# Kernel optimization log

Hardware: AMD Instinct MI355X
Metric: run time of the kernel (lower is better)

## Reference

```python
import jax, jax.numpy as jnp
import numpy as np

HEADS = 8
DIM_HEAD = 64
NH = 16
NW = 16
SCALE = DIM_HEAD ** -0.5


def _avg2x2(a):
    # 2x2 average pool, stride 1, over axes 1,2 of [B,H,W,C] (== unfold+mean in torch)
    return (a[:, :-1, :-1] + a[:, 1:, :-1] + a[:, :-1, 1:] + a[:, 1:, 1:]) * 0.25


def _split_heads(t):
    B, n, _ = t.shape
    return t.reshape(B, n, HEADS, DIM_HEAD).transpose(0, 2, 1, 3)  # b h n d


def setup_inputs() -> dict:
    key = jax.random.key(0)
    ks = jax.random.split(key, 5)
    B, n, dim = 64, 482, 512
    inner = HEADS * DIM_HEAD
    return {
        "x": jax.random.normal(ks[0], (B, n, dim), jnp.float32),
        "mask": jax.random.normal(ks[1], (B, n, dim), jnp.float32),
        "W_qkv": jax.random.normal(ks[2], (3 * inner, dim), jnp.float32) * 0.02,
        "W_out": jax.random.normal(ks[3], (dim, inner), jnp.float32) * 0.02,
        "b_out": jax.random.normal(ks[4], (dim,), jnp.float32) * 0.02,
    }


def reference(x, mask, W_qkv, W_out, b_out):
    sg = jax.lax.stop_gradient
    B, n, dim = x.shape
    inner = HEADS * DIM_HEAD
    nHW = NH * NW            # 256
    nb = (NH - 1) * (NW - 1)  # 225

    # qkv projection
    qkv = x @ W_qkv.T                              # [B,n,3*inner]
    q, k, v = (
        _split_heads(t) for t in jnp.split(qkv, 3, axis=-1)
    )

    # mask path (no grad)
    mask_ = sg(mask)
    updated = (jnp.mean(mask_[:, 1:], axis=-1, keepdims=True) > 0.0).astype(x.dtype)
    updated = jnp.concatenate([jnp.ones_like(updated[:, :1]), updated], axis=1)  # [B,n,1]
    qkv_m = mask_ @ jnp.abs(sg(W_qkv)).T
    q_m, k_m, v_m = (_split_heads(t) for t in jnp.split(qkv_m, 3, axis=-1))
    q_m = q_m / (1e-6 + jnp.max(q_m, axis=2, keepdims=True))
    k_m = k_m / (1e-6 + jnp.max(k_m, axis=2, keepdims=True))
    v_m = v_m / (1e-6 + jnp.max(v_m, axis=2, keepdims=True))
    q_m, k_m, v_m = sg(q_m), sg(k_m), sg(v_m)

    # mask-modulated attention
    dots = jnp.einsum('bhnd,bhmd->bhnm', q * q_m, k * k_m) * SCALE
    attn = jax.nn.softmax(dots, axis=-1)
    out = jnp.einsum('bhnm,bhmd->bhnd', attn, v_m * v)
    out = out.transpose(0, 2, 1, 3).reshape(B, n, inner) * updated

    m = jnp.einsum('bhnm,bhmd->bhnd', sg(attn), v_m)
    m = sg(m.transpose(0, 2, 1, 3).reshape(B, n, inner) * updated)

    # overlap blending (is_overlap=True)
    inv_tail = 1.0 - updated[:, -nb:]
    inv_grid = 1.0 - updated[:, 1:nHW + 1]

    out_bridge = _avg2x2(out[:, 1:nHW + 1].reshape(B, NH, NW, inner)).reshape(B, nb, inner) * inv_tail
    out_origin = jnp.pad(out[:, -nb:].reshape(B, NH - 1, NW - 1, inner),
                         ((0, 0), (1, 1), (1, 1), (0, 0)))
    out_origin = _avg2x2(out_origin).reshape(B, nHW, inner) * inv_grid

    m_bridge = _avg2x2(m[:, 1:nHW + 1].reshape(B, NH, NW, inner)).reshape(B, nb, inner) * inv_tail
    m_origin = jnp.pad(m[:, -nb:].reshape(B, NH - 1, NW - 1, inner),
                       ((0, 0), (1, 1), (1, 1), (0, 0)))
    m_origin = _avg2x2(m_origin).reshape(B, nHW, inner) * inv_grid

    out = out.at[:, 1:nHW + 1].add(out_origin).at[:, -nb:].add(out_bridge)
    m = sg(m.at[:, 1:nHW + 1].add(m_origin).at[:, -nb:].add(m_bridge))

    # nearest-neighbor interpolation of mask means (no grad)
    mm = jnp.mean(m[:, 1:], axis=-1, keepdims=True)          # [B,n-1,1]
    a = mm[:, :nHW].reshape(B, 1, NH, NW)
    inter = jnp.repeat(jnp.repeat(a, 16, axis=2), 16, axis=3)  # [B,1,256,256]
    b = mm[:, -nb:].reshape(B, 1, NH - 1, NW - 1)
    inter_shift = jnp.repeat(jnp.repeat(b, 16, axis=2), 16, axis=3)  # [B,1,240,240]
    inter = inter.at[:, :, 8:-8, 8:-8].set((inter[:, :, 8:-8, 8:-8] + inter_shift) * 0.5)
    inter = sg(inter)

    m = sg(m @ jnp.abs(sg(W_out)).T)

    out_final = out @ W_out.T + b_out
    return out_final, m, inter
```

## Files before the change

kernel.cpp:

```cpp
#include <hip/hip_runtime.h>

#define B_      64
#define NSEQ    482
#define DIM     512
#define HEADS_  8
#define HD      64
#define QKV3    1536
#define NPAD    512
#define MROWS   (B_ * NSEQ)
#define GT      4096

typedef __bf16 v8bf __attribute__((ext_vector_type(8)));
typedef float  v4f  __attribute__((ext_vector_type(4)));
typedef unsigned int v4u __attribute__((ext_vector_type(4)));

typedef __attribute__((address_space(1))) const unsigned short gu16;
typedef __attribute__((address_space(3))) unsigned short lu16;

__device__ __forceinline__ unsigned short f2bf(float f) {
    unsigned u = __float_as_uint(f);
    u += 0x7fffu + ((u >> 16) & 1u);
    return (unsigned short)(u >> 16);
}
__device__ __forceinline__ float bf2f(unsigned short h) {
    return __uint_as_float(((unsigned)h) << 16);
}
__device__ __forceinline__ v8bf vabs8(v8bf x) {
    v4u u;
    __builtin_memcpy(&u, &x, 16);
    u &= (v4u){0x7fff7fffu, 0x7fff7fffu, 0x7fff7fffu, 0x7fff7fffu};
    v8bf r;
    __builtin_memcpy(&r, &u, 16);
    return r;
}

__global__ void k_cvt(const float* __restrict__ s, unsigned short* __restrict__ d, int n4) {
    int i = blockIdx.x * 256 + threadIdx.x;
    if (i < n4) {
        float4 v = ((const float4*)s)[i];
        ushort4 o;
        o.x = f2bf(v.x); o.y = f2bf(v.y); o.z = f2bf(v.z); o.w = f2bf(v.w);
        ((ushort4*)d)[i] = o;
    }
}

__global__ __launch_bounds__(256) void k_cvtmask(const float* __restrict__ mask,
                                                 unsigned short* __restrict__ mb,
                                                 float* __restrict__ upd) {
    int row = blockIdx.x * 4 + (threadIdx.x >> 6);
    int lane = threadIdx.x & 63;
    const float4* p = (const float4*)(mask + (size_t)row * DIM);
    ushort4* d = (ushort4*)(mb + (size_t)row * DIM);
    float s = 0.f;
    #pragma unroll
    for (int j = 0; j < 2; j++) {
        float4 v = p[j * 64 + lane];
        ushort4 o;
        o.x = f2bf(v.x); o.y = f2bf(v.y); o.z = f2bf(v.z); o.w = f2bf(v.w);
        d[j * 64 + lane] = o;
        s += v.x + v.y + v.z + v.w;
    }
    #pragma unroll
    for (int off = 32; off; off >>= 1) s += __shfl_xor(s, off);
    if (lane == 0) {
        int i = row % NSEQ;
        upd[row] = (i == 0) ? 1.f : ((s > 0.f) ? 1.f : 0.f);
    }
}

__global__ __launch_bounds__(256, 2) void k_gemm2(const unsigned short* __restrict__ A1,
                                                  const unsigned short* __restrict__ A2,
                                                  const unsigned short* __restrict__ Bw,
                                                  unsigned short* __restrict__ C1b,
                                                  unsigned short* __restrict__ C2b,
                                                  float* __restrict__ C1f,
                                                  float* __restrict__ C2f,
                                                  const float* __restrict__ bias,
                                                  int N, int K) {
    __shared__ __align__(16) unsigned short As1[3 * GT];
    __shared__ __align__(16) unsigned short As2[3 * GT];
    __shared__ __align__(16) unsigned short Bs[3 * GT];
    int tid = threadIdx.x;
    int lane = tid & 63, w = tid >> 6;
    int wm = w & 1, wn = w >> 1;
    int quad = lane >> 4, m16 = lane & 15;

    int nbx = gridDim.x, nwg = nbx * gridDim.y;
    int id = blockIdx.y * nbx + blockIdx.x;
    int q = nwg >> 3, r = nwg & 7;
    int xcd = id & 7, sub = id >> 3;
    int nid = (xcd < r ? xcd * (q + 1) : r * (q + 1) + (xcd - r) * q) + sub;
    int m0 = (nid / nbx) * 128, n0 = (nid % nbx) * 128;

    int srow = w * 16 + (lane >> 2);
    int scol = ((lane & 3) ^ ((lane >> 2) & 3)) * 8;
    const unsigned short* gA10 = &A1[(size_t)(m0 + srow) * K + scol];
    const unsigned short* gA11 = &A1[(size_t)(m0 + 64 + srow) * K + scol];
    const unsigned short* gA20 = &A2[(size_t)(m0 + srow) * K + scol];
    const unsigned short* gA21 = &A2[(size_t)(m0 + 64 + srow) * K + scol];
    const unsigned short* gB0  = &Bw[(size_t)(n0 + srow) * K + scol];
    const unsigned short* gB1  = &Bw[(size_t)(n0 + 64 + srow) * K + scol];
    lu16* lA10 = (lu16*)&As1[w * 512];
    lu16* lA11 = (lu16*)&As1[2048 + w * 512];
    lu16* lA20 = (lu16*)&As2[w * 512];
    lu16* lA21 = (lu16*)&As2[2048 + w * 512];
    lu16* lB0  = (lu16*)&Bs[w * 512];
    lu16* lB1  = (lu16*)&Bs[2048 + w * 512];

    v4f acc1[4][4], acc2[4][4];
    #pragma unroll
    for (int i = 0; i < 4; i++)
        #pragma unroll
        for (int j = 0; j < 4; j++) {
            acc1[i][j] = (v4f){0.f, 0.f, 0.f, 0.f};
            acc2[i][j] = (v4f){0.f, 0.f, 0.f, 0.f};
        }

    auto STAGE = [&](int bo, int s) {
        int ko = s << 5;
        __builtin_amdgcn_global_load_lds((gu16*)(gA10 + ko), lA10 + bo, 16, 0, 0);
        __builtin_amdgcn_global_load_lds((gu16*)(gA11 + ko), lA11 + bo, 16, 0, 0);
        __builtin_amdgcn_global_load_lds((gu16*)(gA20 + ko), lA20 + bo, 16, 0, 0);
        __builtin_amdgcn_global_load_lds((gu16*)(gA21 + ko), lA21 + bo, 16, 0, 0);
        __builtin_amdgcn_global_load_lds((gu16*)(gB0  + ko), lB0  + bo, 16, 0, 0);
        __builtin_amdgcn_global_load_lds((gu16*)(gB1  + ko), lB1  + bo, 16, 0, 0);
    };
    int csw = (quad ^ (m16 & 3)) << 3;
    auto COMPUTE = [&](int bo) {
        v8bf a1[4], a2[4];
        #pragma unroll
        for (int i = 0; i < 4; i++) {
            a1[i] = *(const v8bf*)&As1[bo + (wm * 64 + i * 16 + m16) * 32 + csw];
            a2[i] = *(const v8bf*)&As2[bo + (wm * 64 + i * 16 + m16) * 32 + csw];
        }
        #pragma unroll
        for (int j = 0; j < 4; j++) {
            v8bf bf = *(const v8bf*)&Bs[bo + (wn * 64 + j * 16 + m16) * 32 + csw];
            v8bf ba = vabs8(bf);
            #pragma unroll
            for (int i = 0; i < 4; i++) {
                acc1[i][j] = __builtin_amdgcn_mfma_f32_16x16x32_bf16(a1[i], bf, acc1[i][j], 0, 0, 0);
                acc2[i][j] = __builtin_amdgcn_mfma_f32_16x16x32_bf16(a2[i], ba, acc2[i][j], 0, 0, 0);
            }
        }
    };

    int steps = K >> 5;
    STAGE(0, 0);
    STAGE(GT, 1);
    int b0 = 0, b1 = GT, b2 = 2 * GT;
    for (int s = 0; s < steps; ++s) {
        if (s < steps - 1) asm volatile("s_waitcnt vmcnt(6)" ::: "memory");
        else               asm volatile("s_waitcnt vmcnt(0)" ::: "memory");
        __builtin_amdgcn_s_barrier();
        __builtin_amdgcn_sched_barrier(0);
        if (s + 2 < steps) STAGE(b2, s + 2);
        COMPUTE(b0);
        int t = b0; b0 = b1; b1 = b2; b2 = t;
    }
    __syncthreads();

    if (C1f) {
        #pragma unroll
        for (int j = 0; j < 4; j++) {
            int col = n0 + wn * 64 + j * 16 + m16;
            float bi = bias ? bias[col] : 0.f;
            #pragma unroll
            for (int i = 0; i < 4; i++) {
                int rowb = m0 + wm * 64 + i * 16 + quad * 4;
                #pragma unroll
                for (int r = 0; r < 4; r++) {
                    size_t off = (size_t)(rowb + r) * N + col;
                    C1f[off] = acc1[i][j][r] + bi;
                    C2f[off] = acc2[i][j][r];
                }
            }
        }
    } else {
        unsigned short* wbuf = &As1[w * 1024];
        int rr = lane >> 2;
        int c0 = ((lane & 3) * 2) ^ ((rr >> 1) & 7);
        size_t colb = n0 + wn * 64 + (lane & 3) * 16;
        #pragma unroll
        for (int i = 0; i < 4; i++) {
            #pragma unroll
            for (int j = 0; j < 4; j++)
                #pragma unroll
                for (int r = 0; r < 4; r++) {
                    int row = quad * 4 + r;
                    int e = j * 16 + m16;
                    int es = ((((e >> 3) ^ ((row >> 1) & 7)) << 3) | (e & 7));
                    wbuf[row * 64 + es] = f2bf(acc1[i][j][r]);
                }
            int4 p0 = *(const int4*)&wbuf[rr * 64 + c0 * 8];
            int4 p1 = *(const int4*)&wbuf[rr * 64 + (c0 ^ 1) * 8];
            size_t off0 = (size_t)(m0 + wm * 64 + i * 16 + rr) * N + colb;
            *(int4*)&C1b[off0] = p0;
            *(int4*)&C1b[off0 + 8] = p1;
        }
        #pragma unroll
        for (int i = 0; i < 4; i++) {
            #pragma unroll
            for (int j = 0; j < 4; j++)
                #pragma unroll
                for (int r = 0; r < 4; r++) {
                    int row = quad * 4 + r;
                    int e = j * 16 + m16;
                    int es = ((((e >> 3) ^ ((row >> 1) & 7)) << 3) | (e & 7));
                    wbuf[row * 64 + es] = f2bf(acc2[i][j][r]);
                }
            int4 p0 = *(const int4*)&wbuf[rr * 64 + c0 * 8];
            int4 p1 = *(const int4*)&wbuf[rr * 64 + (c0 ^ 1) * 8];
            size_t off0 = (size_t)(m0 + wm * 64 + i * 16 + rr) * N + colb;
            *(int4*)&C2b[off0] = p0;
            *(int4*)&C2b[off0 + 8] = p1;
        }
    }
}

__global__ void k_colmax(const unsigned short* __restrict__ qm, float* __restrict__ invsc) {
    int b = blockIdx.x;
    int c = blockIdx.y * 256 + threadIdx.x;
    const unsigned short* p = qm + (size_t)b * NSEQ * QKV3 + c;
    float mx = -1e30f;
    for (int i = 0; i < NSEQ; i++) mx = fmaxf(mx, bf2f(p[(size_t)i * QKV3]));
    invsc[b * QKV3 + c] = 1.f / (1e-6f + mx);
}

__global__ __launch_bounds__(256) void k_build(const unsigned short* __restrict__ qkv,
                                               const unsigned short* __restrict__ qm,
                                               const float* __restrict__ invsc,
                                               unsigned short* __restrict__ QQ,
                                               unsigned short* __restrict__ KK,
                                               unsigned short* __restrict__ VVt,
                                               unsigned short* __restrict__ VMt) {
    __shared__ unsigned short tv[64][72];
    __shared__ unsigned short tm[64][72];
    int tid = threadIdx.x;
    int dd = tid & 63, il = tid >> 6;
    int it = blockIdx.x, h = blockIdx.y, b = blockIdx.z;
    int i0 = it * 64;
    size_t bh = (size_t)(b * HEADS_ + h);
    int c = h * HD + dd;
    float invq = invsc[b * QKV3 + c] * 0.125f;
    float invk = invsc[b * QKV3 + 512 + c];
    float invv = invsc[b * QKV3 + 1024 + c];
    #pragma unroll 4
    for (int p = 0; p < 16; p++) {
        int li = p * 4 + il;
        int i = i0 + li;
        unsigned short oq = 0, ok = 0, ov = 0, om = 0;
        if (i < NSEQ) {
            size_t base = ((size_t)(b * NSEQ + i)) * QKV3 + c;
            float q  = bf2f(qkv[base]),        qv = bf2f(qm[base]);
            float kk = bf2f(qkv[base + 512]),  kv = bf2f(qm[base + 512]);
            float vv = bf2f(qkv[base + 1024]), vm = bf2f(qm[base + 1024]);
            oq = f2bf(q * qv * invq);
            ok = f2bf(kk * kv * invk);
            float vmn = vm * invv;
            ov = f2bf(vv * vmn);
            om = f2bf(vmn);
        }
        QQ[(bh * NPAD + i) * HD + dd] = oq;
        KK[(bh * NPAD + i) * HD + dd] = ok;
        tv[li][dd] = ov;
        tm[li][dd] = om;
    }
    __syncthreads();
    #pragma unroll 4
    for (int p = 0; p < 16; p++) {
        int dr = p * 4 + il;
        VVt[(bh * HD + dr) * NPAD + i0 + dd] = tv[dd][dr];
        VMt[(bh * HD + dr) * NPAD + i0 + dd] = tm[dd][dr];
    }
}

__global__ __launch_bounds__(256, 3) void k_attn(const unsigned short* __restrict__ QQ,
                                                 const unsigned short* __restrict__ KK,
                                                 const unsigned short* __restrict__ VVt,
                                                 const unsigned short* __restrict__ VMt,
                                                 const float* __restrict__ upd,
                                                 float* __restrict__ OUT1,
                                                 float* __restrict__ M1) {
    __shared__ __align__(16) unsigned short Ks[2][32 * 72];
    __shared__ __align__(16) unsigned short Vs[2][64 * 40];
    __shared__ __align__(16) unsigned short Ms[2][64 * 40];
    __shared__ __align__(16) unsigned short Ps[4][32 * 40];

    int tid = threadIdx.x;
    int w = tid >> 6, lane = tid & 63;
    int quad = lane >> 4, m16 = lane & 15;
    int id = (blockIdx.z * 8 + blockIdx.y) * 4 + blockIdx.x;
    int nid = (id & 7) * 256 + (id >> 3);
    int b = nid >> 5, h = (nid >> 2) & 7;
    int q0 = (nid & 3) * 128 + w * 32;
    size_t bh = (size_t)(b * HEADS_ + h);

    v8bf aq[2][2];
    #pragma unroll
    for (int s = 0; s < 2; s++) {
        const unsigned short* qb = &QQ[(bh * NPAD + q0 + s * 16 + m16) * HD];
        aq[s][0] = *(const v8bf*)&qb[quad * 8];
        aq[s][1] = *(const v8bf*)&qb[32 + quad * 8];
    }

    v4f vacc[2][4], macc[2][4];
    #pragma unroll
    for (int s = 0; s < 2; s++)
        #pragma unroll
        for (int dt = 0; dt < 4; dt++) {
            vacc[s][dt] = (v4f){0.f, 0.f, 0.f, 0.f};
            macc[s][dt] = (v4f){0.f, 0.f, 0.f, 0.f};
        }
    float lrun[2][4];
    #pragma unroll
    for (int s = 0; s < 2; s++)
        #pragma unroll
        for (int r = 0; r < 4; r++) lrun[s][r] = 0.f;

    const unsigned short* gK = &KK[bh * NPAD * HD + tid * 8];
    const unsigned short* gV = &VVt[(bh * HD + (tid >> 2)) * NPAD + (tid & 3) * 8];
    const unsigned short* gM = &VMt[(bh * HD + (tid >> 2)) * NPAD + (tid & 3) * 8];
    int oK = (tid >> 3) * 72 + (tid & 7) * 8;
    int oV = (tid >> 2) * 40 + (tid & 3) * 8;
    unsigned short* Pw = &Ps[w][0];

    int4 rk = *(const int4*)gK;
    int4 rv = *(const int4*)gV;
    int4 rm = *(const int4*)gM;

    for (int ic = 0; ic < 16; ++ic) {
        int buf = ic & 1;
        *(int4*)&Ks[buf][oK] = rk;
        *(int4*)&Vs[buf][oV] = rv;
        *(int4*)&Ms[buf][oV] = rm;
        if (ic < 15) {
            rk = *(const int4*)(gK + (ic + 1) * 32 * HD);
            rv = *(const int4*)(gV + (ic + 1) * 32);
            rm = *(const int4*)(gM + (ic + 1) * 32);
        }
        __syncthreads();

        v8bf kf[2][2];
        #pragma unroll
        for (int t = 0; t < 2; t++) {
            kf[t][0] = *(const v8bf*)&Ks[buf][(t * 16 + m16) * 72 + quad * 8];
            kf[t][1] = *(const v8bf*)&Ks[buf][(t * 16 + m16) * 72 + 32 + quad * 8];
        }
        v4f S[2][2];
        #pragma unroll
        for (int s = 0; s < 2; s++)
            #pragma unroll
            for (int t = 0; t < 2; t++) {
                v4f a = (v4f){0.f, 0.f, 0.f, 0.f};
                a = __builtin_amdgcn_mfma_f32_16x16x32_bf16(aq[s][0], kf[t][0], a, 0, 0, 0);
                a = __builtin_amdgcn_mfma_f32_16x16x32_bf16(aq[s][1], kf[t][1], a, 0, 0, 0);
                S[s][t] = a;
            }

        int i0 = ic * 32;
        if (i0 + 32 > NSEQ) {
            bool x0 = (i0 + m16) >= NSEQ;
            bool x1 = (i0 + 16 + m16) >= NSEQ;
            #pragma unroll
            for (int s = 0; s < 2; s++)
                #pragma unroll
                for (int r = 0; r < 4; r++) {
                    if (x0) S[s][0][r] = -1e30f;
                    if (x1) S[s][1][r] = -1e30f;
                }
        }

        #pragma unroll
        for (int s = 0; s < 2; s++)
            #pragma unroll
            for (int r = 0; r < 4; r++) {
                float e0 = __expf(S[s][0][r]);
                float e1 = __expf(S[s][1][r]);
                lrun[s][r] += e0 + e1;
                Pw[(s * 16 + quad * 4 + r) * 40 + m16] = f2bf(e0);
                Pw[(s * 16 + quad * 4 + r) * 40 + 16 + m16] = f2bf(e1);
            }

        v8bf ap[2];
        ap[0] = *(const v8bf*)&Pw[m16 * 40 + quad * 8];
        ap[1] = *(const v8bf*)&Pw[(16 + m16) * 40 + quad * 8];

        #pragma unroll
        for (int dt = 0; dt < 4; dt++) {
            v8bf bv = *(const v8bf*)&Vs[buf][(dt * 16 + m16) * 40 + quad * 8];
            v8bf bm = *(const v8bf*)&Ms[buf][(dt * 16 + m16) * 40 + quad * 8];
            #pragma unroll
            for (int s = 0; s < 2; s++) {
                vacc[s][dt] = __builtin_amdgcn_mfma_f32_16x16x32_bf16(ap[s], bv, vacc[s][dt], 0, 0, 0);
                macc[s][dt] = __builtin_amdgcn_mfma_f32_16x16x32_bf16(ap[s], bm, macc[s][dt], 0, 0, 0);
            }
        }
    }

    #pragma unroll
    for (int s = 0; s < 2; s++)
        #pragma unroll
        for (int r = 0; r < 4; r++) {
            float sum = lrun[s][r];
            sum += __shfl_xor(sum, 1);
            sum += __shfl_xor(sum, 2);
            sum += __shfl_xor(sum, 4);
            sum += __shfl_xor(sum, 8);
            float iv = 1.f / sum;
            int iq = q0 + s * 16 + quad * 4 + r;
            if (iq < NSEQ) {
                float u = upd[b * NSEQ + iq] * iv;
                size_t off = ((size_t)(b * NSEQ + iq)) * DIM + h * HD + m16;
                #pragma unroll
                for (int dt = 0; dt < 4; dt++) {
                    OUT1[off + dt * 16] = vacc[s][dt][r] * u;
                    M1[off + dt * 16]   = macc[s][dt][r] * u;
                }
            }
        }
}

__global__ __launch_bounds__(256) void k_blend(const float* __restrict__ O1,
                                               const float* __restrict__ Mm,
                                               const float* __restrict__ upd,
                                               unsigned short* __restrict__ O2,
                                               unsigned short* __restrict__ M2,
                                               float* __restrict__ mm) {
    int blk = blockIdx.x;
    int b = blk / NSEQ, i = blk - b * NSEQ;
    int tid = threadIdx.x;
    size_t rb = (size_t)blk * DIM;
    int ns = 0;
    size_t src[4];
    float wgt = 0.f;
    if (i >= 1) {
        wgt = 0.25f * (1.f - upd[blk]);
        if (wgt != 0.f) {
            if (i <= 256) {
                int g = i - 1, gy = g >> 4, gx = g & 15;
                #pragma unroll
                for (int dy = 0; dy < 2; dy++)
                    #pragma unroll
                    for (int dx = 0; dx < 2; dx++) {
                        int sy = gy - 1 + dy, sx = gx - 1 + dx;
                        if (sy >= 0 && sy < 15 && sx >= 0 && sx < 15)
                            src[ns++] = ((size_t)(b * NSEQ + 257 + sy * 15 + sx)) * DIM;
                    }
            } else {
                int t = i - 257, ty = t / 15, tx = t - ty * 15;
                #pragma unroll
                for (int dy = 0; dy < 2; dy++)
                    #pragma unroll
                    for (int dx = 0; dx < 2; dx++)
                        src[ns++] = ((size_t)(b * NSEQ + 1 + (ty + dy) * 16 + (tx + dx))) * DIM;
            }
        }
    }
    float msum = 0.f;
    for (int c = tid; c < DIM; c += 256) {
        float o = O1[rb + c], m = Mm[rb + c];
        float ao = 0.f, am = 0.f;
        for (int s = 0; s < ns; s++) { ao += O1[src[s] + c]; am += Mm[src[s] + c]; }
        o += wgt * ao;
        m += wgt * am;
        O2[rb + c] = f2bf(o);
        M2[rb + c] = f2bf(m);
        msum += m;
    }
    #pragma unroll
    for (int off = 32; off; off >>= 1) msum += __shfl_xor(msum, off);
    __shared__ float red[4];
    if ((tid & 63) == 0) red[tid >> 6] = msum;
    __syncthreads();
    if (tid == 0 && i >= 1)
        mm[b * 481 + i - 1] = (red[0] + red[1] + red[2] + red[3]) * (1.f / 512.f);
}

__global__ void k_inter(const float* __restrict__ mm, float* __restrict__ dst) {
    int idx = blockIdx.x * 256 + threadIdx.x;
    int b = idx >> 16, rem = idx & 65535;
    int y = rem >> 8, x = rem & 255;
    const float* mb = mm + b * 481;
    float v = mb[((y >> 4) << 4) + (x >> 4)];
    if (y >= 8 && y < 248 && x >= 8 && x < 248)
        v = 0.5f * (v + mb[256 + ((y - 8) >> 4) * 15 + ((x - 8) >> 4)]);
    dst[idx] = v;
}

extern "C" void kernel_launch(void* const* d_in, const int* in_sizes, int n_in,
                              void* d_out, int out_size, void* d_ws, size_t ws_size,
                              hipStream_t stream) {
    const float* x    = (const float*)d_in[0];
    const float* mask = (const float*)d_in[1];
    const float* Wqkv = (const float*)d_in[2];
    const float* Wout = (const float*)d_in[3];
    const float* bout = (const float*)d_in[4];
    float* out = (float*)d_out;

    char* ws = (char*)d_ws;
    size_t o = 0;
    auto alloc = [&](size_t bytes) -> char* {
        char* r = ws + o;
        o += (bytes + 255) & ~(size_t)255;
        return r;
    };
    unsigned short* xb    = (unsigned short*)alloc((size_t)MROWS * DIM * 2);
    unsigned short* maskb = (unsigned short*)alloc((size_t)MROWS * DIM * 2);
    unsigned short* Wb    = (unsigned short*)alloc((size_t)QKV3 * DIM * 2);
    unsigned short* Wob   = (unsigned short*)alloc((size_t)DIM * DIM * 2);
    unsigned short* qkvb  = (unsigned short*)alloc((size_t)MROWS * QKV3 * 2);
    unsigned short* qkvmb = (unsigned short*)alloc((size_t)MROWS * QKV3 * 2);
    float* upd  = (float*)alloc((size_t)MROWS * 4);
    float* invs = (float*)alloc((size_t)B_ * QKV3 * 4);
    float* mm   = (float*)alloc((size_t)B_ * 481 * 4);
    unsigned short* QQ  = (unsigned short*)alloc((size_t)B_ * HEADS_ * NPAD * HD * 2);
    unsigned short* KK  = (unsigned short*)alloc((size_t)B_ * HEADS_ * NPAD * HD * 2);
    unsigned short* VVt = (unsigned short*)alloc((size_t)B_ * HEADS_ * NPAD * HD * 2);
    unsigned short* VMt = (unsigned short*)alloc((size_t)B_ * HEADS_ * NPAD * HD * 2);
    float* OUT1 = (float*)qkvb;
    float* M1p  = (float*)qkvmb;
    unsigned short* O2 = xb;
    unsigned short* M2 = maskb;

    k_cvt<<<(MROWS * DIM / 4) / 256, 256, 0, stream>>>(x, xb, MROWS * DIM / 4);
    k_cvtmask<<<MROWS / 4, 256, 0, stream>>>(mask, maskb, upd);
    k_cvt<<<(QKV3 * DIM / 4) / 256, 256, 0, stream>>>(Wqkv, Wb, QKV3 * DIM / 4);
    k_cvt<<<(DIM * DIM / 4) / 256, 256, 0, stream>>>(Wout, Wob, DIM * DIM / 4);

    dim3 g1(QKV3 / 128, MROWS / 128);
    k_gemm2<<<g1, 256, 0, stream>>>(xb, maskb, Wb, qkvb, qkvmb,
                                    nullptr, nullptr, nullptr, QKV3, DIM);

    k_colmax<<<dim3(B_, QKV3 / 256), 256, 0, stream>>>(qkvmb, invs);
    k_build<<<dim3(8, HEADS_, B_), 256, 0, stream>>>(qkvb, qkvmb, invs, QQ, KK, VVt, VMt);

    k_attn<<<dim3(4, HEADS_, B_), 256, 0, stream>>>(QQ, KK, VVt, VMt, upd, OUT1, M1p);

    k_blend<<<MROWS, 256, 0, stream>>>(OUT1, M1p, upd, O2, M2, mm);
    k_inter<<<(B_ * 65536) / 256, 256, 0, stream>>>(mm, out + (size_t)2 * MROWS * DIM);

    dim3 g2(DIM / 128, MROWS / 128);
    k_gemm2<<<g2, 256, 0, stream>>>(O2, M2, Wob, nullptr, nullptr,
                                    out, out + (size_t)MROWS * DIM, bout, DIM, DIM);
}
```

Before: 754.3 us.

## Split dual GEMM across two 4-wave groups in 512-thread blocks

Restructures the fused dual GEMM (x·W and mask·|W|) so each 512-thread block has two groups of four waves. Each group computes one of the two products with a single 4x4 accumulator set, instead of every wave computing both. The aim is to halve per-wave accumulator pressure and raise wave-level parallelism while still sharing the B tile in LDS. In exchange it drops the XOR LDS swizzle, so reads may hit bank conflicts. It also sets launch bounds of (512,4), which may force heavy register limits or spills, and LDS use may cap occupancy well below that hint anyway.

```diff
diff --git a/kernel.cpp b/kernel.cpp
--- a/kernel.cpp
+++ b/kernel.cpp
@@ -68,7 +68,7 @@
     }
 }
 
-__global__ __launch_bounds__(256, 2) void k_gemm2(const unsigned short* __restrict__ A1,
+__global__ __launch_bounds__(512, 4) void k_gemm2(const unsigned short* __restrict__ A1,
                                                   const unsigned short* __restrict__ A2,
                                                   const unsigned short* __restrict__ Bw,
                                                   unsigned short* __restrict__ C1b,
@@ -82,7 +82,8 @@
     __shared__ __align__(16) unsigned short Bs[3 * GT];
     int tid = threadIdx.x;
     int lane = tid & 63, w = tid >> 6;
-    int wm = w & 1, wn = w >> 1;
+    int grp = w >> 2;
+    int wm = (w >> 1) & 1, wn = w & 1;
     int quad = lane >> 4, m16 = lane & 15;
 
     int nbx = gridDim.x, nwg = nbx * gridDim.y;
@@ -92,56 +93,39 @@
     int nid = (xcd < r ? xcd * (q + 1) : r * (q + 1) + (xcd - r) * q) + sub;
     int m0 = (nid / nbx) * 128, n0 = (nid % nbx) * 128;
 
-    int srow = w * 16 + (lane >> 2);
-    int scol = ((lane & 3) ^ ((lane >> 2) & 3)) * 8;
-    const unsigned short* gA10 = &A1[(size_t)(m0 + srow) * K + scol];
-    const unsigned short* gA11 = &A1[(size_t)(m0 + 64 + srow) * K + scol];
-    const unsigned short* gA20 = &A2[(size_t)(m0 + srow) * K + scol];
-    const unsigned short* gA21 = &A2[(size_t)(m0 + 64 + srow) * K + scol];
-    const unsigned short* gB0  = &Bw[(size_t)(n0 + srow) * K + scol];
-    const unsigned short* gB1  = &Bw[(size_t)(n0 + 64 + srow) * K + scol];
-    lu16* lA10 = (lu16*)&As1[w * 512];
-    lu16* lA11 = (lu16*)&As1[2048 + w * 512];
-    lu16* lA20 = (lu16*)&As2[w * 512];
-    lu16* lA21 = (lu16*)&As2[2048 + w * 512];
-    lu16* lB0  = (lu16*)&Bs[w * 512];
-    lu16* lB1  = (lu16*)&Bs[2048 + w * 512];
-
-    v4f acc1[4][4], acc2[4][4];
+    int srow = tid >> 2, scol = (tid & 3) * 8;
+    const unsigned short* gA1 = &A1[(size_t)(m0 + srow) * K + scol];
+    const unsigned short* gA2 = &A2[(size_t)(m0 + srow) * K + scol];
+    const unsigned short* gB  = &Bw[(size_t)(n0 + srow) * K + scol];
+    lu16* lA1 = (lu16*)&As1[w * 512];
+    lu16* lA2 = (lu16*)&As2[w * 512];
+    lu16* lB  = (lu16*)&Bs[w * 512];
+
+    v4f acc[4][4];
     #pragma unroll
     for (int i = 0; i < 4; i++)
         #pragma unroll
-        for (int j = 0; j < 4; j++) {
-            acc1[i][j] = (v4f){0.f, 0.f, 0.f, 0.f};
-            acc2[i][j] = (v4f){0.f, 0.f, 0.f, 0.f};
-        }
+        for (int j = 0; j < 4; j++) acc[i][j] = (v4f){0.f, 0.f, 0.f, 0.f};
 
     auto STAGE = [&](int bo, int s) {
         int ko = s << 5;
-        __builtin_amdgcn_global_load_lds((gu16*)(gA10 + ko), lA10 + bo, 16, 0, 0);
-        __builtin_amdgcn_global_load_lds((gu16*)(gA11 + ko), lA11 + bo, 16, 0, 0);
-        __builtin_amdgcn_global_load_lds((gu16*)(gA20 + ko), lA20 + bo, 16, 0, 0);
-        __builtin_amdgcn_global_load_lds((gu16*)(gA21 + ko), lA21 + bo, 16, 0, 0);
-        __builtin_amdgcn_global_load_lds((gu16*)(gB0  + ko), lB0  + bo, 16, 0, 0);
-        __builtin_amdgcn_global_load_lds((gu16*)(gB1  + ko), lB1  + bo, 16, 0, 0);
+        __builtin_amdgcn_global_load_lds((gu16*)(gA1 + ko), lA1 + bo, 16, 0, 0);
+        __builtin_amdgcn_global_load_lds((gu16*)(gA2 + ko), lA2 + bo, 16, 0, 0);
+        __builtin_amdgcn_global_load_lds((gu16*)(gB  + ko), lB  + bo, 16, 0, 0);
     };
-    int csw = (quad ^ (m16 & 3)) << 3;
+    const unsigned short* Ams = grp ? As2 : As1;
     auto COMPUTE = [&](int bo) {
-        v8bf a1[4], a2[4];
-        #pragma unroll
-        for (int i = 0; i < 4; i++) {
-            a1[i] = *(const v8bf*)&As1[bo + (wm * 64 + i * 16 + m16) * 32 + csw];
-            a2[i] = *(const v8bf*)&As2[bo + (wm * 64 + i * 16 + m16) * 32 + csw];
-        }
+        v8bf a[4];
+        #pragma unroll
+        for (int i = 0; i < 4; i++)
+            a[i] = *(const v8bf*)&Ams[bo + (wm * 64 + i * 16 + m16) * 32 + quad * 8];
         #pragma unroll
         for (int j = 0; j < 4; j++) {
-            v8bf bf = *(const v8bf*)&Bs[bo + (wn * 64 + j * 16 + m16) * 32 + csw];
-            v8bf ba = vabs8(bf);
-            #pragma unroll
-            for (int i = 0; i < 4; i++) {
-                acc1[i][j] = __builtin_amdgcn_mfma_f32_16x16x32_bf16(a1[i], bf, acc1[i][j], 0, 0, 0);
-                acc2[i][j] = __builtin_amdgcn_mfma_f32_16x16x32_bf16(a2[i], ba, acc2[i][j], 0, 0, 0);
-            }
+            v8bf b = *(const v8bf*)&Bs[bo + (wn * 64 + j * 16 + m16) * 32 + quad * 8];
+            if (grp) b = vabs8(b);
+            #pragma unroll
+            for (int i = 0; i < 4; i++)
+                acc[i][j] = __builtin_amdgcn_mfma_f32_16x16x32_bf16(a[i], b, acc[i][j], 0, 0, 0);
         }
     };
 
@@ -150,7 +134,7 @@
     STAGE(GT, 1);
     int b0 = 0, b1 = GT, b2 = 2 * GT;
     for (int s = 0; s < steps; ++s) {
-        if (s < steps - 1) asm volatile("s_waitcnt vmcnt(6)" ::: "memory");
+        if (s < steps - 1) asm volatile("s_waitcnt vmcnt(3)" ::: "memory");
         else               asm volatile("s_waitcnt vmcnt(0)" ::: "memory");
         __builtin_amdgcn_s_barrier();
         __builtin_amdgcn_sched_barrier(0);
@@ -161,22 +145,23 @@
     __syncthreads();
 
     if (C1f) {
+        float* Cf = grp ? C2f : C1f;
         #pragma unroll
         for (int j = 0; j < 4; j++) {
             int col = n0 + wn * 64 + j * 16 + m16;
-            float bi = bias ? bias[col] : 0.f;
+            float bi = (bias && !grp) ? bias[col] : 0.f;
             #pragma unroll
             for (int i = 0; i < 4; i++) {
                 int rowb = m0 + wm * 64 + i * 16 + quad * 4;
                 #pragma unroll
                 for (int r = 0; r < 4; r++) {
                     size_t off = (size_t)(rowb + r) * N + col;
-                    C1f[off] = acc1[i][j][r] + bi;
-                    C2f[off] = acc2[i][j][r];
+                    Cf[off] = acc[i][j][r] + bi;
                 }
             }
         }
     } else {
+        unsigned short* Cb = grp ? C2b : C1b;
         unsigned short* wbuf = &As1[w * 1024];
         int rr = lane >> 2;
         int c0 = ((lane & 3) * 2) ^ ((rr >> 1) & 7);
@@ -190,30 +175,13 @@
                     int row = quad * 4 + r;
                     int e = j * 16 + m16;
                     int es = ((((e >> 3) ^ ((row >> 1) & 7)) << 3) | (e & 7));
-                    wbuf[row * 64 + es] = f2bf(acc1[i][j][r]);
+                    wbuf[row * 64 + es] = f2bf(acc[i][j][r]);
                 }
             int4 p0 = *(const int4*)&wbuf[rr * 64 + c0 * 8];
             int4 p1 = *(const int4*)&wbuf[rr * 64 + (c0 ^ 1) * 8];
             size_t off0 = (size_t)(m0 + wm * 64 + i * 16 + rr) * N + colb;
-            *(int4*)&C1b[off0] = p0;
-            *(int4*)&C1b[off0 + 8] = p1;
-        }
-        #pragma unroll
-        for (int i = 0; i < 4; i++) {
-            #pragma unroll
-            for (int j = 0; j < 4; j++)
-                #pragma unroll
-                for (int r = 0; r < 4; r++) {
-                    int row = quad * 4 + r;
-                    int e = j * 16 + m16;
-                    int es = ((((e >> 3) ^ ((row >> 1) & 7)) << 3) | (e & 7));
-                    wbuf[row * 64 + es] = f2bf(acc2[i][j][r]);
-                }
-            int4 p0 = *(const int4*)&wbuf[rr * 64 + c0 * 8];
-            int4 p1 = *(const int4*)&wbuf[rr * 64 + (c0 ^ 1) * 8];
-            size_t off0 = (size_t)(m0 + wm * 64 + i * 16 + rr) * N + colb;
-            *(int4*)&C2b[off0] = p0;
-            *(int4*)&C2b[off0 + 8] = p1;
+            *(int4*)&Cb[off0] = p0;
+            *(int4*)&Cb[off0 + 8] = p1;
         }
     }
 }
@@ -529,7 +497,7 @@
     k_cvt<<<(DIM * DIM / 4) / 256, 256, 0, stream>>>(Wout, Wob, DIM * DIM / 4);
 
     dim3 g1(QKV3 / 128, MROWS / 128);
-    k_gemm2<<<g1, 256, 0, stream>>>(xb, maskb, Wb, qkvb, qkvmb,
+    k_gemm2<<<g1, 512, 0, stream>>>(xb, maskb, Wb, qkvb, qkvmb,
                                     nullptr, nullptr, nullptr, QKV3, DIM);
 
     k_colmax<<<dim3(B_, QKV3 / 256), 256, 0, stream>>>(qkvmb, invs);
@@ -541,6 +509,6 @@
     k_inter<<<(B_ * 65536) / 256, 256, 0, stream>>>(mm, out + (size_t)2 * MROWS * DIM);
 
     dim3 g2(DIM / 128, MROWS / 128);
-    k_gemm2<<<g2, 256, 0, stream>>>(O2, M2, Wob, nullptr, nullptr,
+    k_gemm2<<<g2, 512, 0, stream>>>(O2, M2, Wob, nullptr, nullptr,
                                     out, out + (size_t)MROWS * DIM, bout, DIM, DIM);
 }
```

Measured after the change: 757.7 us. Within noise of the previous version (+0.5%).
